# Performance work log

Hardware: AMD Instinct MI355X
Metric: run time of the kernel (lower is better)

The kernel has to match this reference:

```python
import jax, jax.numpy as jnp
import numpy as np

T, B, I, H = 2048, 512, 1, 64


def setup_inputs() -> dict:
    key = jax.random.key(0)
    ks = jax.random.split(key, 8)
    s_in = 1.0 / np.sqrt(H)  # torch RNN/Linear init scale (uniform bound)
    return {
        "x": jax.random.normal(ks[0], (T, B, I), dtype=jnp.float32),
        "h": jax.random.normal(ks[1], (1, B, H), dtype=jnp.float32),
        "W_ih": jax.random.uniform(ks[2], (H, I), jnp.float32, -s_in, s_in),
        "W_hh": jax.random.uniform(ks[3], (H, H), jnp.float32, -s_in, s_in),
        "b_ih": jax.random.uniform(ks[4], (H,), jnp.float32, -s_in, s_in),
        "b_hh": jax.random.uniform(ks[5], (H,), jnp.float32, -s_in, s_in),
        "W_lin": jax.random.uniform(ks[6], (1, H), jnp.float32, -s_in, s_in),
        "b_lin": jax.random.uniform(ks[7], (1,), jnp.float32, -s_in, s_in),
    }


def reference(x, h, W_ih, W_hh, b_ih, b_hh, W_lin, b_lin):
    # tanh RNN: h_t = tanh(x_t W_ih^T + b_ih + h_{t-1} W_hh^T + b_hh)
    h0 = h[0]  # [B, H]
    # precompute input projection for all timesteps: [T, B, H]
    xp = jnp.einsum('tbi,hi->tbh', x, W_ih) + b_ih + b_hh

    def step(h_prev, xp_t):
        h_new = jnp.tanh(xp_t + h_prev @ W_hh.T)
        return h_new, h_new

    h_last, hs = jax.lax.scan(step, h0, xp)  # hs: [T, B, H]
    y = jnp.einsum('tbh,oh->tbo', hs, W_lin) + b_lin  # [T, B, 1]
    return y, h_last[None]  # h_n: [1, B, H]
```

## Files before the change

### kernel.cpp

```cpp
#include <hip/hip_runtime.h>

#define TT 2048
#define BB 512
#define HH 64
#define HIST 64
#define HPAD 68

typedef float f32x2 __attribute__((ext_vector_type(2)));
typedef float f32x4 __attribute__((ext_vector_type(4)));

#define FMA2(a, b, c) __builtin_elementwise_fma((a), (b), (c))
#define LO2(q) __builtin_shufflevector((q), (q), 0, 1)
#define HI2(q) __builtin_shufflevector((q), (q), 2, 3)

#define DPP_ADD(v, ctrl) \
    ((v) + __int_as_float(__builtin_amdgcn_update_dpp(0, __float_as_int(v), (ctrl), 0xF, 0xF, false)))

__global__ __launch_bounds__(64, 1) void rnn_fused(
    const float* __restrict__ x,
    const float* __restrict__ h0,
    const float* __restrict__ Wih,
    const float* __restrict__ Whh,
    const float* __restrict__ bih,
    const float* __restrict__ bhh,
    const float* __restrict__ Wlin,
    const float* __restrict__ blin,
    float* __restrict__ y,
    float* __restrict__ hN)
{
    __shared__ float wsh[HH * HH];
    __shared__ float xsh[TT + 4];
    __shared__ __align__(16) float hist[HIST][HPAD];
    __shared__ __align__(16) float wlin_sh[HH];

    const int b    = blockIdx.x;
    const int lane = threadIdx.x;
    const int hl   = lane >> 2;
    const int ks   = lane & 3;
    const int d    = ks * 16 + hl;

    for (int i = lane; i < HH * HH; i += 64) wsh[i] = Whh[i];
    for (int i = lane; i < TT; i += 64)      xsh[i] = x[(size_t)i * BB + b];
    if (lane < 4) xsh[TT + lane] = 0.f;
    wlin_sh[lane] = Wlin[lane];

    const float KSC = 2.885390081777927f;

    f32x2 wr[32];
#pragma unroll
    for (int g = 0; g < 4; ++g) {
        const float* row = &wsh[(g * 16 + hl) * HH + ks * 16];
#pragma unroll
        for (int i = 0; i < 8; ++i) {
            wr[g * 8 + i][0] = row[2 * i + 0] * KSC;
            wr[g * 8 + i][1] = row[2 * i + 1] * KSC;
        }
    }
    const float wihs  = Wih[d] * KSC;
    const float biass = (bih[d] + bhh[d]) * KSC;
    const float bl    = blin[0];

    hist[HIST - 1][d] = h0[(size_t)b * HH + d];
    float hval = 0.f;
    float xw   = fmaf(xsh[0], wihs, biass);

#pragma unroll 1
    for (int tc = 0; tc < TT; tc += HIST) {
#pragma unroll 2
        for (int ti = 0; ti < HIST; ++ti) {
            const int t  = tc + ti;
            const int rs = (ti + HIST - 1) & (HIST - 1);

            const f32x4* hp = reinterpret_cast<const f32x4*>(&hist[rs][ks * 16]);
            const f32x4 p0 = hp[0], p1 = hp[1], p2 = hp[2], p3 = hp[3];
            const f32x2 d0 = LO2(p0), d1 = HI2(p0), d2 = LO2(p1), d3 = HI2(p1);
            const f32x2 d4 = LO2(p2), d5 = HI2(p2), d6 = LO2(p3), d7 = HI2(p3);

            f32x2 g0a = {0.f, 0.f}, g0b = {0.f, 0.f};
            f32x2 g1a = {0.f, 0.f}, g1b = {0.f, 0.f};
            f32x2 g2a = {0.f, 0.f}, g2b = {0.f, 0.f};
            f32x2 g3a = {0.f, 0.f}, g3b = {0.f, 0.f};
            g0a = FMA2(d0, wr[0],  g0a); g0b = FMA2(d1, wr[1],  g0b);
            g0a = FMA2(d2, wr[2],  g0a); g0b = FMA2(d3, wr[3],  g0b);
            g0a = FMA2(d4, wr[4],  g0a); g0b = FMA2(d5, wr[5],  g0b);
            g0a = FMA2(d6, wr[6],  g0a); g0b = FMA2(d7, wr[7],  g0b);
            g1a = FMA2(d0, wr[8],  g1a); g1b = FMA2(d1, wr[9],  g1b);
            g1a = FMA2(d2, wr[10], g1a); g1b = FMA2(d3, wr[11], g1b);
            g1a = FMA2(d4, wr[12], g1a); g1b = FMA2(d5, wr[13], g1b);
            g1a = FMA2(d6, wr[14], g1a); g1b = FMA2(d7, wr[15], g1b);
            g2a = FMA2(d0, wr[16], g2a); g2b = FMA2(d1, wr[17], g2b);
            g2a = FMA2(d2, wr[18], g2a); g2b = FMA2(d3, wr[19], g2b);
            g2a = FMA2(d4, wr[20], g2a); g2b = FMA2(d5, wr[21], g2b);
            g2a = FMA2(d6, wr[22], g2a); g2b = FMA2(d7, wr[23], g2b);
            g3a = FMA2(d0, wr[24], g3a); g3b = FMA2(d1, wr[25], g3b);
            g3a = FMA2(d2, wr[26], g3a); g3b = FMA2(d3, wr[27], g3b);
            g3a = FMA2(d4, wr[28], g3a); g3b = FMA2(d5, wr[29], g3b);
            g3a = FMA2(d6, wr[30], g3a); g3b = FMA2(d7, wr[31], g3b);

            const f32x2 h0v = g0a + g0b, h1v = g1a + g1b;
            const f32x2 h2v = g2a + g2b, h3v = g3a + g3b;
            float s0 = h0v[0] + h0v[1];
            float s1 = h1v[0] + h1v[1];
            float s2 = h2v[0] + h2v[1];
            float s3 = h3v[0] + h3v[1];

            s0 = DPP_ADD(s0, 0xB1); s0 = DPP_ADD(s0, 0x4E);
            s1 = DPP_ADD(s1, 0xB1); s1 = DPP_ADD(s1, 0x4E);
            s2 = DPP_ADD(s2, 0xB1); s2 = DPP_ADD(s2, 0x4E);
            s3 = DPP_ADD(s3, 0xB1); s3 = DPP_ADD(s3, 0x4E);

            const float sA = (ks & 1) ? s1 : s0;
            const float sB = (ks & 1) ? s3 : s2;
            const float s  = (ks & 2) ? sB : sA;

            const float acc = s + xw;

            const float e2 = __builtin_amdgcn_exp2f(acc);
            const float r  = __builtin_amdgcn_rcpf(e2 + 1.0f);
            hval = fmaf(-2.0f, r, 1.0f);

            hist[ti][d] = hval;

            xw = fmaf(xsh[t + 1], wihs, biass);
        }

        {
            const f32x4* rp = reinterpret_cast<const f32x4*>(&hist[lane][0]);
            const f32x4* wl = reinterpret_cast<const f32x4*>(&wlin_sh[0]);
            f32x2 a2 = {0.f, 0.f};
#pragma unroll
            for (int i = 0; i < 16; ++i) {
                const f32x4 qq = rp[i];
                const f32x4 qw = wl[i];
                a2 = FMA2(LO2(qq), LO2(qw), a2);
                a2 = FMA2(HI2(qq), HI2(qw), a2);
            }
            y[(size_t)(tc + lane) * BB + b] = a2[0] + a2[1] + bl;
        }
    }

    hN[(size_t)b * HH + d] = hval;
}

extern "C" void kernel_launch(void* const* d_in, const int* in_sizes, int n_in,
                              void* d_out, int out_size, void* d_ws, size_t ws_size,
                              hipStream_t stream) {
    const float* x    = (const float*)d_in[0];
    const float* h0   = (const float*)d_in[1];
    const float* Wih  = (const float*)d_in[2];
    const float* Whh  = (const float*)d_in[3];
    const float* bih  = (const float*)d_in[4];
    const float* bhh  = (const float*)d_in[5];
    const float* Wlin = (const float*)d_in[6];
    const float* blin = (const float*)d_in[7];

    float* y  = (float*)d_out;
    float* hN = (float*)d_out + TT * BB;

    rnn_fused<<<dim3(BB), dim3(64), 0, stream>>>(x, h0, Wih, Whh, bih, bhh, Wlin, blin, y, hN);
}
```

Before: 381.4 us.

## Interleave two independent batch recurrences per wavefront with padded history slots

Each 64-thread block now processes two batch elements, interleaving their recurrence steps so one chain's dependent matvec, DPP reduction and tanh can overlap with the other's, which hides latency on the serial recurrence. Hidden states are stored in a padded slot layout (20 floats per k-slice) and reloaded into registers right after the write, so the next step's LDS read comes from a fixed location. W_hh is read directly from global memory as float4 rather than staged through shared memory. Launching half as many blocks lowers occupancy, and the per-block serial work doubles, so the outcome depends on whether ILP gains outweigh the loss of parallelism across CUs.

```diff
diff --git a/kernel.cpp b/kernel.cpp
--- a/kernel.cpp
+++ b/kernel.cpp
@@ -4,7 +4,7 @@
 #define BB 512
 #define HH 64
 #define HIST 64
-#define HPAD 68
+#define HPAD 80
 
 typedef float f32x2 __attribute__((ext_vector_type(2)));
 typedef float f32x4 __attribute__((ext_vector_type(4)));
@@ -28,118 +28,140 @@
     float* __restrict__ y,
     float* __restrict__ hN)
 {
-    __shared__ float wsh[HH * HH];
-    __shared__ float xsh[TT + 4];
-    __shared__ __align__(16) float hist[HIST][HPAD];
-    __shared__ __align__(16) float wlin_sh[HH];
+    __shared__ float xsh[2][TT + 4];
+    __shared__ __align__(16) float hist[2][HIST][HPAD];
+    __shared__ __align__(16) float wlin_sh[HPAD];
 
-    const int b    = blockIdx.x;
+    const int b0   = 2 * blockIdx.x;
+    const int b1   = b0 + 1;
     const int lane = threadIdx.x;
     const int hl   = lane >> 2;
     const int ks   = lane & 3;
     const int d    = ks * 16 + hl;
+    const int slot = ks * 20 + hl;
 
-    for (int i = lane; i < HH * HH; i += 64) wsh[i] = Whh[i];
-    for (int i = lane; i < TT; i += 64)      xsh[i] = x[(size_t)i * BB + b];
-    if (lane < 4) xsh[TT + lane] = 0.f;
-    wlin_sh[lane] = Wlin[lane];
+    float* hflat = &hist[0][0][0];
+    for (int i = lane; i < 2 * HIST * HPAD; i += 64) hflat[i] = 0.f;
+    for (int i = lane; i < HPAD; i += 64) wlin_sh[i] = 0.f;
+
+    for (int i = lane; i < TT; i += 64) {
+        xsh[0][i] = x[(size_t)i * BB + b0];
+        xsh[1][i] = x[(size_t)i * BB + b1];
+    }
+    if (lane < 4) { xsh[0][TT + lane] = 0.f; xsh[1][TT + lane] = 0.f; }
 
     const float KSC = 2.885390081777927f;
 
     f32x2 wr[32];
 #pragma unroll
     for (int g = 0; g < 4; ++g) {
-        const float* row = &wsh[(g * 16 + hl) * HH + ks * 16];
-#pragma unroll
-        for (int i = 0; i < 8; ++i) {
-            wr[g * 8 + i][0] = row[2 * i + 0] * KSC;
-            wr[g * 8 + i][1] = row[2 * i + 1] * KSC;
-        }
+        const float4* rowp = reinterpret_cast<const float4*>(Whh + (g * 16 + hl) * HH + ks * 16);
+        const float4 v0 = rowp[0], v1 = rowp[1], v2 = rowp[2], v3 = rowp[3];
+        wr[g * 8 + 0] = f32x2{v0.x * KSC, v0.y * KSC};
+        wr[g * 8 + 1] = f32x2{v0.z * KSC, v0.w * KSC};
+        wr[g * 8 + 2] = f32x2{v1.x * KSC, v1.y * KSC};
+        wr[g * 8 + 3] = f32x2{v1.z * KSC, v1.w * KSC};
+        wr[g * 8 + 4] = f32x2{v2.x * KSC, v2.y * KSC};
+        wr[g * 8 + 5] = f32x2{v2.z * KSC, v2.w * KSC};
+        wr[g * 8 + 6] = f32x2{v3.x * KSC, v3.y * KSC};
+        wr[g * 8 + 7] = f32x2{v3.z * KSC, v3.w * KSC};
     }
     const float wihs  = Wih[d] * KSC;
     const float biass = (bih[d] + bhh[d]) * KSC;
     const float bl    = blin[0];
 
-    hist[HIST - 1][d] = h0[(size_t)b * HH + d];
-    float hval = 0.f;
-    float xw   = fmaf(xsh[0], wihs, biass);
+    wlin_sh[slot] = Wlin[d];
+
+    hist[0][HIST - 1][slot] = h0[(size_t)b0 * HH + d];
+    hist[1][HIST - 1][slot] = h0[(size_t)b1 * HH + d];
+
+    const f32x4* pr0 = reinterpret_cast<const f32x4*>(&hist[0][HIST - 1][ks * 20]);
+    const f32x4* pr1 = reinterpret_cast<const f32x4*>(&hist[1][HIST - 1][ks * 20]);
+    f32x4 A0 = pr0[0], A1 = pr0[1], A2 = pr0[2], A3 = pr0[3];
+    f32x4 B0 = pr1[0], B1 = pr1[1], B2 = pr1[2], B3 = pr1[3];
+
+    float xw0 = fmaf(xsh[0][0], wihs, biass);
+    float xw1 = fmaf(xsh[1][0], wihs, biass);
+    float hv0 = 0.f, hv1 = 0.f;
+
+#define COL_STEP(C, R0, R1, R2, R3, HV, XW)                                        \
+    {                                                                              \
+        const f32x2 e0 = LO2(R0), e1 = HI2(R0), e2 = LO2(R1), e3 = HI2(R1);        \
+        const f32x2 e4 = LO2(R2), e5 = HI2(R2), e6 = LO2(R3), e7 = HI2(R3);        \
+        f32x2 g0a = {0.f, 0.f}, g0b = {0.f, 0.f};                                  \
+        f32x2 g1a = {0.f, 0.f}, g1b = {0.f, 0.f};                                  \
+        f32x2 g2a = {0.f, 0.f}, g2b = {0.f, 0.f};                                  \
+        f32x2 g3a = {0.f, 0.f}, g3b = {0.f, 0.f};                                  \
+        g0a = FMA2(e0, wr[0],  g0a); g0b = FMA2(e1, wr[1],  g0b);                  \
+        g0a = FMA2(e2, wr[2],  g0a); g0b = FMA2(e3, wr[3],  g0b);                  \
+        g0a = FMA2(e4, wr[4],  g0a); g0b = FMA2(e5, wr[5],  g0b);                  \
+        g0a = FMA2(e6, wr[6],  g0a); g0b = FMA2(e7, wr[7],  g0b);                  \
+        g1a = FMA2(e0, wr[8],  g1a); g1b = FMA2(e1, wr[9],  g1b);                  \
+        g1a = FMA2(e2, wr[10], g1a); g1b = FMA2(e3, wr[11], g1b);                  \
+        g1a = FMA2(e4, wr[12], g1a); g1b = FMA2(e5, wr[13], g1b);                  \
+        g1a = FMA2(e6, wr[14], g1a); g1b = FMA2(e7, wr[15], g1b);                  \
+        g2a = FMA2(e0, wr[16], g2a); g2b = FMA2(e1, wr[17], g2b);                  \
+        g2a = FMA2(e2, wr[18], g2a); g2b = FMA2(e3, wr[19], g2b);                  \
+        g2a = FMA2(e4, wr[20], g2a); g2b = FMA2(e5, wr[21], g2b);                  \
+        g2a = FMA2(e6, wr[22], g2a); g2b = FMA2(e7, wr[23], g2b);                  \
+        g3a = FMA2(e0, wr[24], g3a); g3b = FMA2(e1, wr[25], g3b);                  \
+        g3a = FMA2(e2, wr[26], g3a); g3b = FMA2(e3, wr[27], g3b);                  \
+        g3a = FMA2(e4, wr[28], g3a); g3b = FMA2(e5, wr[29], g3b);                  \
+        g3a = FMA2(e6, wr[30], g3a); g3b = FMA2(e7, wr[31], g3b);                  \
+        const f32x2 h0v = g0a + g0b, h1v = g1a + g1b;                              \
+        const f32x2 h2v = g2a + g2b, h3v = g3a + g3b;                              \
+        float s0 = h0v[0] + h0v[1];                                                \
+        float s1 = h1v[0] + h1v[1];                                                \
+        float s2 = h2v[0] + h2v[1];                                                \
+        float s3 = h3v[0] + h3v[1];                                                \
+        s0 = DPP_ADD(s0, 0xB1); s0 = DPP_ADD(s0, 0x4E);                            \
+        s1 = DPP_ADD(s1, 0xB1); s1 = DPP_ADD(s1, 0x4E);                            \
+        s2 = DPP_ADD(s2, 0xB1); s2 = DPP_ADD(s2, 0x4E);                            \
+        s3 = DPP_ADD(s3, 0xB1); s3 = DPP_ADD(s3, 0x4E);                            \
+        const float sA = (ks & 1) ? s1 : s0;                                       \
+        const float sB = (ks & 1) ? s3 : s2;                                       \
+        const float s  = (ks & 2) ? sB : sA;                                       \
+        const float acc = s + (XW);                                                \
+        const float ex = __builtin_amdgcn_exp2f(acc);                              \
+        const float rc = __builtin_amdgcn_rcpf(ex + 1.0f);                         \
+        (HV) = fmaf(-2.0f, rc, 1.0f);                                              \
+        hist[C][ti][slot] = (HV);                                                  \
+        const f32x4* rp_ = reinterpret_cast<const f32x4*>(&hist[C][ti][ks * 20]);  \
+        R0 = rp_[0]; R1 = rp_[1]; R2 = rp_[2]; R3 = rp_[3];                        \
+        (XW) = fmaf(xsh[C][t + 1], wihs, biass);                                   \
+    }
 
 #pragma unroll 1
     for (int tc = 0; tc < TT; tc += HIST) {
 #pragma unroll 2
         for (int ti = 0; ti < HIST; ++ti) {
-            const int t  = tc + ti;
-            const int rs = (ti + HIST - 1) & (HIST - 1);
-
-            const f32x4* hp = reinterpret_cast<const f32x4*>(&hist[rs][ks * 16]);
-            const f32x4 p0 = hp[0], p1 = hp[1], p2 = hp[2], p3 = hp[3];
-            const f32x2 d0 = LO2(p0), d1 = HI2(p0), d2 = LO2(p1), d3 = HI2(p1);
-            const f32x2 d4 = LO2(p2), d5 = HI2(p2), d6 = LO2(p3), d7 = HI2(p3);
-
-            f32x2 g0a = {0.f, 0.f}, g0b = {0.f, 0.f};
-            f32x2 g1a = {0.f, 0.f}, g1b = {0.f, 0.f};
-            f32x2 g2a = {0.f, 0.f}, g2b = {0.f, 0.f};
-            f32x2 g3a = {0.f, 0.f}, g3b = {0.f, 0.f};
-            g0a = FMA2(d0, wr[0],  g0a); g0b = FMA2(d1, wr[1],  g0b);
-            g0a = FMA2(d2, wr[2],  g0a); g0b = FMA2(d3, wr[3],  g0b);
-            g0a = FMA2(d4, wr[4],  g0a); g0b = FMA2(d5, wr[5],  g0b);
-            g0a = FMA2(d6, wr[6],  g0a); g0b = FMA2(d7, wr[7],  g0b);
-            g1a = FMA2(d0, wr[8],  g1a); g1b = FMA2(d1, wr[9],  g1b);
-            g1a = FMA2(d2, wr[10], g1a); g1b = FMA2(d3, wr[11], g1b);
-            g1a = FMA2(d4, wr[12], g1a); g1b = FMA2(d5, wr[13], g1b);
-            g1a = FMA2(d6, wr[14], g1a); g1b = FMA2(d7, wr[15], g1b);
-            g2a = FMA2(d0, wr[16], g2a); g2b = FMA2(d1, wr[17], g2b);
-            g2a = FMA2(d2, wr[18], g2a); g2b = FMA2(d3, wr[19], g2b);
-            g2a = FMA2(d4, wr[20], g2a); g2b = FMA2(d5, wr[21], g2b);
-            g2a = FMA2(d6, wr[22], g2a); g2b = FMA2(d7, wr[23], g2b);
-            g3a = FMA2(d0, wr[24], g3a); g3b = FMA2(d1, wr[25], g3b);
-            g3a = FMA2(d2, wr[26], g3a); g3b = FMA2(d3, wr[27], g3b);
-            g3a = FMA2(d4, wr[28], g3a); g3b = FMA2(d5, wr[29], g3b);
-            g3a = FMA2(d6, wr[30], g3a); g3b = FMA2(d7, wr[31], g3b);
-
-            const f32x2 h0v = g0a + g0b, h1v = g1a + g1b;
-            const f32x2 h2v = g2a + g2b, h3v = g3a + g3b;
-            float s0 = h0v[0] + h0v[1];
-            float s1 = h1v[0] + h1v[1];
-            float s2 = h2v[0] + h2v[1];
-            float s3 = h3v[0] + h3v[1];
-
-            s0 = DPP_ADD(s0, 0xB1); s0 = DPP_ADD(s0, 0x4E);
-            s1 = DPP_ADD(s1, 0xB1); s1 = DPP_ADD(s1, 0x4E);
-            s2 = DPP_ADD(s2, 0xB1); s2 = DPP_ADD(s2, 0x4E);
-            s3 = DPP_ADD(s3, 0xB1); s3 = DPP_ADD(s3, 0x4E);
-
-            const float sA = (ks & 1) ? s1 : s0;
-            const float sB = (ks & 1) ? s3 : s2;
-            const float s  = (ks & 2) ? sB : sA;
-
-            const float acc = s + xw;
-
-            const float e2 = __builtin_amdgcn_exp2f(acc);
-            const float r  = __builtin_amdgcn_rcpf(e2 + 1.0f);
-            hval = fmaf(-2.0f, r, 1.0f);
-
-            hist[ti][d] = hval;
-
-            xw = fmaf(xsh[t + 1], wihs, biass);
+            const int t = tc + ti;
+            COL_STEP(0, A0, A1, A2, A3, hv0, xw0)
+            COL_STEP(1, B0, B1, B2, B3, hv1, xw1)
         }
 
         {
-            const f32x4* rp = reinterpret_cast<const f32x4*>(&hist[lane][0]);
             const f32x4* wl = reinterpret_cast<const f32x4*>(&wlin_sh[0]);
-            f32x2 a2 = {0.f, 0.f};
+            const f32x4* r0 = reinterpret_cast<const f32x4*>(&hist[0][lane][0]);
+            const f32x4* r1 = reinterpret_cast<const f32x4*>(&hist[1][lane][0]);
+            f32x2 a0 = {0.f, 0.f}, a1 = {0.f, 0.f};
 #pragma unroll
-            for (int i = 0; i < 16; ++i) {
-                const f32x4 qq = rp[i];
+            for (int i = 0; i < HPAD / 4; ++i) {
                 const f32x4 qw = wl[i];
-                a2 = FMA2(LO2(qq), LO2(qw), a2);
-                a2 = FMA2(HI2(qq), HI2(qw), a2);
+                const f32x4 q0 = r0[i];
+                const f32x4 q1 = r1[i];
+                a0 = FMA2(LO2(q0), LO2(qw), a0);
+                a0 = FMA2(HI2(q0), HI2(qw), a0);
+                a1 = FMA2(LO2(q1), LO2(qw), a1);
+                a1 = FMA2(HI2(q1), HI2(qw), a1);
             }
-            y[(size_t)(tc + lane) * BB + b] = a2[0] + a2[1] + bl;
+            y[(size_t)(tc + lane) * BB + b0] = a0[0] + a0[1] + bl;
+            y[(size_t)(tc + lane) * BB + b1] = a1[0] + a1[1] + bl;
         }
     }
 
-    hN[(size_t)b * HH + d] = hval;
+    hN[(size_t)b0 * HH + d] = hv0;
+    hN[(size_t)b1 * HH + d] = hv1;
 }
 
 extern "C" void kernel_launch(void* const* d_in, const int* in_sizes, int n_in,
@@ -157,5 +179,5 @@
     float* y  = (float*)d_out;
     float* hN = (float*)d_out + TT * BB;
 
-    rnn_fused<<<dim3(BB), dim3(64), 0, stream>>>(x, h0, Wih, Whh, bih, bhh, Wlin, blin, y, hN);
+    rnn_fused<<<dim3(BB / 2), dim3(64), 0, stream>>>(x, h0, Wih, Whh, bih, bhh, Wlin, blin, y, hN);
 }
```

Result: slower. 606.4 us (+59.0%).
